# Kernel optimization log

Hardware: AMD Instinct MI355X
Metric: run time of the kernel (lower is better)

The kernel has to match this reference:

```python
import jax, jax.numpy as jnp
import numpy as np

B = 65536          # batch
E = 512            # embedding_dim
SL = 128           # speed_latent_dim
H = 256            # hidden_size
NB = 6             # num_branch
D = E + SL         # 640, branch input dim


def _linear_init(k, din, dout):
    bound = 1.0 / np.sqrt(din)
    kw, kb = jax.random.split(k)
    W = jax.random.uniform(kw, (din, dout), minval=-bound, maxval=bound, dtype=jnp.float32)
    b = jax.random.uniform(kb, (dout,), minval=-bound, maxval=bound, dtype=jnp.float32)
    return W, b


def setup_inputs() -> dict:
    key = jax.random.key(0)
    ks = jax.random.split(key, 10)
    embedding = jax.random.normal(ks[0], (B, E), dtype=jnp.float32)
    speed = jax.random.uniform(ks[1], (B, 1), dtype=jnp.float32)
    command = jax.random.randint(ks[2], (B,), 1, NB + 1)  # values in 1..6

    # speed_in: Linear(1,H) -> ReLU -> Linear(H,SL)
    si_W1, si_b1 = _linear_init(ks[3], 1, H)
    si_W2, si_b2 = _linear_init(ks[4], H, SL)

    # speed_out: Linear(D,H) -> ReLU -> Linear(H,H) -> ReLU -> Linear(H,1)
    so_W1, so_b1 = _linear_init(ks[5], D, H)
    so_W2, so_b2 = _linear_init(ks[6], H, H)
    so_W3, so_b3 = _linear_init(ks[7], H, 1)

    # NB branches, each Linear(D,H)->ReLU->Linear(H,H)->ReLU->Linear(H,3)->Sigmoid
    def mk_branch(k):
        k1, k2, k3 = jax.random.split(k, 3)
        W1, b1 = _linear_init(k1, D, H)
        W2, b2 = _linear_init(k2, H, H)
        W3, b3 = _linear_init(k3, H, 3)
        return W1, b1, W2, b2, W3, b3

    bW1, bb1, bW2, bb2, bW3, bb3 = jax.vmap(mk_branch)(jax.random.split(ks[8], NB))

    return {
        "embedding": embedding, "speed": speed, "command": command,
        "si_W1": si_W1, "si_b1": si_b1, "si_W2": si_W2, "si_b2": si_b2,
        "bW1": bW1, "bb1": bb1, "bW2": bW2, "bb2": bb2, "bW3": bW3, "bb3": bb3,
        "so_W1": so_W1, "so_b1": so_b1, "so_W2": so_W2, "so_b2": so_b2,
        "so_W3": so_W3, "so_b3": so_b3,
    }


def reference(embedding, speed, command,
              si_W1, si_b1, si_W2, si_b2,
              bW1, bb1, bW2, bb2, bW3, bb3,
              so_W1, so_b1, so_W2, so_b2, so_W3, so_b3):
    # speed_in MLP and concat
    s = jax.nn.relu(speed @ si_W1 + si_b1) @ si_W2 + si_b2          # [B, SL]
    emb = jnp.concatenate([embedding, s], axis=1)                    # [B, D]

    # all branches computed densely (as in the torch module), then one-hot mask
    h1 = jax.nn.relu(jnp.einsum('bd,ndh->nbh', emb, bW1) + bb1[:, None, :])   # [NB,B,H]
    h2 = jax.nn.relu(jnp.einsum('nbh,nhk->nbk', h1, bW2) + bb2[:, None, :])   # [NB,B,H]
    out = jax.nn.sigmoid(jnp.einsum('nbk,nko->nbo', h2, bW3) + bb3[:, None, :])  # [NB,B,3]

    mask = (jnp.arange(NB)[:, None] == (command - 1)[None, :]).astype(out.dtype)  # [NB,B]
    control_pred = jnp.sum(out * mask[:, :, None], axis=0)           # [B, 3]

    # speed prediction head
    sp = jax.nn.relu(emb @ so_W1 + so_b1)
    sp = jax.nn.relu(sp @ so_W2 + so_b2)
    speed_pred = sp @ so_W3 + so_b3                                  # [B, 1]

    return control_pred, speed_pred
```

## Files before the change

kernel.cpp:

```cpp
#include <hip/hip_runtime.h>
#include <cstdint>
#include <cstddef>

typedef _Float16 f16;
typedef f16 f16x8 __attribute__((ext_vector_type(8)));
typedef float f32x4 __attribute__((ext_vector_type(4)));

#define B_ROWS 65536
#define TILE_M 128
#define NT_BRANCH 518
#define NT_SPEED 512

constexpr size_t OFF_AF16   = 0;
constexpr size_t SZ_AF16    = (size_t)B_ROWS * 640 * 2;
constexpr size_t OFF_SIW2T  = OFF_AF16 + SZ_AF16;
constexpr size_t SZ_SIW2T   = (size_t)128 * 256 * 2;
constexpr size_t OFF_BW1T   = OFF_SIW2T + SZ_SIW2T;
constexpr size_t SZ_BW1T    = (size_t)6 * 256 * 640 * 2;
constexpr size_t OFF_BW2T   = OFF_BW1T + SZ_BW1T;
constexpr size_t SZ_BW2T    = (size_t)6 * 256 * 256 * 2;
constexpr size_t OFF_SOW1T  = OFF_BW2T + SZ_BW2T;
constexpr size_t SZ_SOW1T   = (size_t)256 * 640 * 2;
constexpr size_t OFF_SOW2T  = OFF_SOW1T + SZ_SOW1T;
constexpr size_t SZ_SOW2T   = (size_t)256 * 256 * 2;
constexpr size_t OFF_BW3T16 = OFF_SOW2T + SZ_SOW2T;
constexpr size_t SZ_BW3T16  = (size_t)6 * 16 * 256 * 2;
constexpr size_t OFF_SOW3T16= OFF_BW3T16 + SZ_BW3T16;
constexpr size_t SZ_SOW3T16 = (size_t)16 * 256 * 2;
constexpr size_t OFF_COUNTS = OFF_SOW3T16 + SZ_SOW3T16;
constexpr size_t OFF_CURSORS= OFF_COUNTS + 256;
constexpr size_t OFF_BINBASE= OFF_CURSORS + 256;
constexpr size_t OFF_TILECMD= OFF_BINBASE + 256;
constexpr size_t OFF_PERM   = OFF_TILECMD + 4352;
constexpr size_t WS_NEEDED  = OFF_PERM + (size_t)NT_BRANCH * TILE_M * 4;

#define MFMA16(a, b, c) __builtin_amdgcn_mfma_f32_16x16x32_f16(a, b, c, 0, 0, 0)
#define BARSYNC() asm volatile("s_waitcnt lgkmcnt(0)\n\ts_barrier" ::: "memory")
#define GLOAD16(gp, lp) __builtin_amdgcn_global_load_lds( \
    (const __attribute__((address_space(1))) void*)(gp),  \
    (__attribute__((address_space(3))) void*)(lp), 16, 0, 0)

__global__ void prep_kernel(const float* __restrict__ siW2,
                            const float* __restrict__ bW1,
                            const float* __restrict__ bW2,
                            const float* __restrict__ soW1,
                            const float* __restrict__ soW2,
                            const float* __restrict__ bW3,
                            const float* __restrict__ soW3,
                            f16* __restrict__ siW2T, f16* __restrict__ bW1T,
                            f16* __restrict__ bW2T, f16* __restrict__ soW1T,
                            f16* __restrict__ soW2T,
                            f16* __restrict__ bW3T16, f16* __restrict__ soW3T16,
                            int* __restrict__ counts, int* __restrict__ cursors,
                            int* __restrict__ perm)
{
    const int bx = blockIdx.x;
    const int tx = threadIdx.x, ty = threadIdx.y;
    const int tid = ty * 32 + tx;
    if (bx >= 1601) {
        const int ib = bx - 1601;
        const int idx = ib * 256 + tid;
        if (idx < NT_BRANCH * TILE_M) perm[idx] = -1;
        if (ib == 0 && tid < 6) { counts[tid] = 0; cursors[tid] = 0; }
        return;
    }
    if (bx == 1600) {
        for (int i = tid; i < 6 * 16 * 256; i += 256) {
            const int c = i >> 12, rem = i & 4095, n = rem >> 8, k = rem & 255;
            bW3T16[i] = (n < 3) ? (f16)bW3[((size_t)c * 256 + k) * 3 + n] : (f16)0;
        }
        for (int i = tid; i < 16 * 256; i += 256) {
            const int n = i >> 8, k = i & 255;
            soW3T16[i] = (n == 0) ? (f16)soW3[k] : (f16)0;
        }
        return;
    }
    const float* in; f16* out; int R, C, lb;
    if (bx < 960)       { int m = bx / 160;        lb = bx - m * 160;       in = bW1 + (size_t)m * 640 * 256; out = bW1T + (size_t)m * 640 * 256; R = 640; C = 256; }
    else if (bx < 1344) { int m = (bx - 960) / 64; lb = (bx - 960) - m * 64; in = bW2 + (size_t)m * 256 * 256; out = bW2T + (size_t)m * 256 * 256; R = 256; C = 256; }
    else if (bx < 1504) { lb = bx - 1344; in = soW1; out = soW1T; R = 640; C = 256; }
    else if (bx < 1568) { lb = bx - 1504; in = soW2; out = soW2T; R = 256; C = 256; }
    else                { lb = bx - 1568; in = siW2; out = siW2T; R = 256; C = 128; }
    const int txt = C >> 5;
    const int c0 = (lb % txt) << 5;
    const int r0 = (lb / txt) << 5;
    __shared__ float tile[32][33];
    #pragma unroll
    for (int i = 0; i < 4; ++i)
        tile[tx][ty + 8 * i] = in[(size_t)(r0 + ty + 8 * i) * C + c0 + tx];
    __syncthreads();
    #pragma unroll
    for (int i = 0; i < 4; ++i)
        out[(size_t)(c0 + ty + 8 * i) * R + r0 + tx] = (f16)tile[ty + 8 * i][tx];
}

__global__ __launch_bounds__(256) void speedin_kernel(
    const float* __restrict__ emb,
    const float* __restrict__ speed,
    const float* __restrict__ siW1, const float* __restrict__ sib1,
    const f16* __restrict__ siW2T, const float* __restrict__ sib2,
    const int* __restrict__ cmd,
    f16* __restrict__ AF16, int* __restrict__ counts)
{
    __shared__ f16 H[64 * 264];
    __shared__ float spd[64];
    __shared__ int h[6];
    const int tid = threadIdx.x;
    const int rb = blockIdx.x * 64;
    if (tid < 6) h[tid] = 0;
    __syncthreads();
    if (tid < 64) {
        spd[tid] = speed[rb + tid];
        atomicAdd(&h[cmd[rb + tid] - 1], 1);
    }
    __syncthreads();
    if (tid < 6 && h[tid] > 0) atomicAdd(&counts[tid], h[tid]);
    {
        const int wv = tid >> 6, ln = tid & 63;
        #pragma unroll 4
        for (int rr = 0; rr < 16; ++rr) {
            const int row = rb + wv * 16 + rr;
            const float* src = emb + (size_t)row * 512 + ln * 8;
            const float4 f0 = ((const float4*)src)[0];
            const float4 f1 = ((const float4*)src)[1];
            f16x8 v;
            v[0] = (f16)f0.x; v[1] = (f16)f0.y; v[2] = (f16)f0.z; v[3] = (f16)f0.w;
            v[4] = (f16)f1.x; v[5] = (f16)f1.y; v[6] = (f16)f1.z; v[7] = (f16)f1.w;
            *(f16x8*)(AF16 + (size_t)row * 640 + ln * 8) = v;
        }
    }
    {
        const float w1 = siW1[tid], b1v = sib1[tid];
        #pragma unroll 4
        for (int r = 0; r < 64; ++r) {
            float hv = spd[r] * w1 + b1v;
            H[r * 264 + tid] = (f16)(hv > 0.f ? hv : 0.f);
        }
    }
    __syncthreads();
    const int w = tid >> 6, lane = tid & 63, lq = lane >> 4, l16 = lane & 15;
    const int nb = w * 32;
    f32x4 acc[4][2];
    #pragma unroll
    for (int mt = 0; mt < 4; ++mt)
        #pragma unroll
        for (int nt = 0; nt < 2; ++nt)
            acc[mt][nt] = (f32x4){0.f, 0.f, 0.f, 0.f};
    for (int ks = 0; ks < 8; ++ks) {
        const int koff = ks * 32 + lq * 8;
        f16x8 af[4], bf[2];
        #pragma unroll
        for (int mt = 0; mt < 4; ++mt)
            af[mt] = *(const f16x8*)(&H[(mt * 16 + l16) * 264 + koff]);
        #pragma unroll
        for (int nt = 0; nt < 2; ++nt)
            bf[nt] = *(const f16x8*)(siW2T + (size_t)(nb + nt * 16 + l16) * 256 + koff);
        #pragma unroll
        for (int mt = 0; mt < 4; ++mt)
            #pragma unroll
            for (int nt = 0; nt < 2; ++nt)
                acc[mt][nt] = MFMA16(af[mt], bf[nt], acc[mt][nt]);
    }
    #pragma unroll
    for (int mt = 0; mt < 4; ++mt)
        #pragma unroll
        for (int nt = 0; nt < 2; ++nt) {
            const int n = nb + nt * 16 + l16;
            const float bv = sib2[n];
            #pragma unroll
            for (int r2 = 0; r2 < 4; ++r2) {
                const int m = mt * 16 + lq * 4 + r2;
                AF16[(size_t)(rb + m) * 640 + 512 + n] = (f16)(acc[mt][nt][r2] + bv);
            }
        }
}

__global__ void plan_kernel(const int* __restrict__ counts,
                            int* __restrict__ binBase, int* __restrict__ tile_cmd) {
    __shared__ int tbase[7];
    if (threadIdx.x == 0) {
        int base = 0, tb = 0;
        for (int c = 0; c < 6; ++c) {
            binBase[c] = base;
            tbase[c] = tb;
            const int nt = (counts[c] + TILE_M - 1) >> 7;
            tb += nt;
            base += nt << 7;
        }
        tbase[6] = tb;
    }
    __syncthreads();
    for (int t = threadIdx.x; t < NT_BRANCH; t += 256) {
        int c = -1;
        #pragma unroll
        for (int j = 0; j < 6; ++j)
            if (t >= tbase[j] && t < tbase[j + 1]) c = j;
        tile_cmd[t] = c;
    }
}

__global__ void place_kernel(const int* __restrict__ cmd,
                             const int* __restrict__ binBase,
                             int* __restrict__ cursors, int* __restrict__ perm) {
    __shared__ int lcnt[6], lbase[6];
    const int tid = threadIdx.x;
    if (tid < 6) lcnt[tid] = 0;
    __syncthreads();
    const int i = blockIdx.x * 256 + tid;
    const int c = cmd[i] - 1;
    const int myr = atomicAdd(&lcnt[c], 1);
    __syncthreads();
    if (tid < 6) lbase[tid] = atomicAdd(&cursors[tid], lcnt[tid]);
    __syncthreads();
    perm[binBase[c] + lbase[c] + myr] = i;
}

__global__ __launch_bounds__(512, 4) void heads_kernel(
    const f16* __restrict__ AF16,
    const int* __restrict__ perm, const int* __restrict__ tile_cmd,
    const f16* __restrict__ bW1T, const f16* __restrict__ bW2T,
    const f16* __restrict__ bW3T16,
    const float* __restrict__ bb1, const float* __restrict__ bb2,
    const float* __restrict__ bb3,
    const f16* __restrict__ soW1T, const f16* __restrict__ soW2T,
    const f16* __restrict__ soW3T16,
    const float* __restrict__ sob1, const float* __restrict__ sob2,
    const float* __restrict__ sob3,
    float* __restrict__ out)
{
    __shared__ f16 smem[33792];
    __shared__ int rowIdx[TILE_M];
    const int bx = blockIdx.x;
    const int tid = threadIdx.x;
    const bool is_speed = (bx >= NT_BRANCH);
    const f16 *W1T, *W2T, *W3T;
    const float *bias1, *bias2, *bias3;
    if (is_speed) {
        const int t = bx - NT_BRANCH;
        if (tid < TILE_M) rowIdx[tid] = t * TILE_M + tid;
        W1T = soW1T; W2T = soW2T; W3T = soW3T16;
        bias1 = sob1; bias2 = sob2; bias3 = sob3;
    } else {
        const int c = tile_cmd[bx];
        if (c < 0) return;
        if (tid < TILE_M) rowIdx[tid] = perm[bx * TILE_M + tid];
        W1T = bW1T + (size_t)c * 256 * 640;
        W2T = bW2T + (size_t)c * 256 * 256;
        W3T = bW3T16 + (size_t)c * 16 * 256;
        bias1 = bb1 + c * 256; bias2 = bb2 + c * 256; bias3 = bb3 + c * 3;
    }
    __syncthreads();

    const int r0 = tid >> 3, j = tid & 7, key = r0 & 7;
    int g0 = rowIdx[r0];      if (g0 < 0) g0 = 0;
    int g1 = rowIdx[r0 + 64]; if (g1 < 0) g1 = 0;
    const f16* srcP0 = AF16 + (size_t)g0 * 640 + (j ^ key) * 8;
    const f16* srcP1 = AF16 + (size_t)g1 * 640 + (j ^ key) * 8;

    const int w = tid >> 6, lane = tid & 63, lq = lane >> 4, l16 = lane & 15;
    const int ldsW = w * 512;
    const int nb = w * 32;
    const f16* brow0 = W1T + (size_t)(nb + l16) * 640;
    const f16* brow1 = W1T + (size_t)(nb + 16 + l16) * 640;

    f32x4 acc[8][2];
    #pragma unroll
    for (int mt = 0; mt < 8; ++mt)
        #pragma unroll
        for (int nt = 0; nt < 2; ++nt)
            acc[mt][nt] = (f32x4){0.f, 0.f, 0.f, 0.f};

    GLOAD16(srcP0,            smem + 0 * 8192 + ldsW);
    GLOAD16(srcP1,            smem + 0 * 8192 + 4096 + ldsW);
    GLOAD16(srcP0 + 64,       smem + 1 * 8192 + ldsW);
    GLOAD16(srcP1 + 64,       smem + 1 * 8192 + 4096 + ldsW);
    asm volatile("s_waitcnt vmcnt(2)\n\ts_barrier" ::: "memory");

    #pragma unroll
    for (int kc = 0; kc < 10; ++kc) {
        const f16* cur = smem + (kc % 3) * 8192;
        f16x8 Bb[2][2];
        #pragma unroll
        for (int ks = 0; ks < 2; ++ks) {
            Bb[ks][0] = *(const f16x8*)(brow0 + kc * 64 + ks * 32 + lq * 8);
            Bb[ks][1] = *(const f16x8*)(brow1 + kc * 64 + ks * 32 + lq * 8);
        }
        if (kc < 8) {
            GLOAD16(srcP0 + (kc + 2) * 64, smem + ((kc + 2) % 3) * 8192 + ldsW);
            GLOAD16(srcP1 + (kc + 2) * 64, smem + ((kc + 2) % 3) * 8192 + 4096 + ldsW);
        }
        #pragma unroll
        for (int ks = 0; ks < 2; ++ks)
            #pragma unroll
            for (int mh = 0; mh < 2; ++mh) {
                f16x8 a[4];
                #pragma unroll
                for (int mt = 0; mt < 4; ++mt) {
                    const int row = mh * 64 + mt * 16 + l16;
                    a[mt] = *(const f16x8*)(cur + row * 64 + ((ks * 4 + lq) ^ (l16 & 7)) * 8);
                }
                #pragma unroll
                for (int mt = 0; mt < 4; ++mt) {
                    acc[mh * 4 + mt][0] = MFMA16(a[mt], Bb[ks][0], acc[mh * 4 + mt][0]);
                    acc[mh * 4 + mt][1] = MFMA16(a[mt], Bb[ks][1], acc[mh * 4 + mt][1]);
                }
            }
        if (kc < 8)
            asm volatile("s_waitcnt vmcnt(2)\n\ts_barrier" ::: "memory");
        else if (kc == 8)
            asm volatile("s_waitcnt vmcnt(4)\n\ts_barrier" ::: "memory");
        else
            BARSYNC();
    }

    const f16* brow2[2];
    #pragma unroll
    for (int nt = 0; nt < 2; ++nt)
        brow2[nt] = W2T + (size_t)(nb + nt * 16 + l16) * 256;
    f16x8 Bd[2][2];
    #pragma unroll
    for (int nt = 0; nt < 2; ++nt)
        Bd[0][nt] = *(const f16x8*)(brow2[nt] + lq * 8);

    #pragma unroll
    for (int mt = 0; mt < 8; ++mt)
        #pragma unroll
        for (int nt = 0; nt < 2; ++nt) {
            const int n = nb + nt * 16 + l16;
            const float bv = bias1[n];
            #pragma unroll
            for (int r2 = 0; r2 < 4; ++r2) {
                const int m = mt * 16 + lq * 4 + r2;
                const float v = acc[mt][nt][r2] + bv;
                smem[m * 264 + n] = (f16)(v > 0.f ? v : 0.f);
            }
            acc[mt][nt] = (f32x4){0.f, 0.f, 0.f, 0.f};
        }
    BARSYNC();

    #pragma unroll
    for (int ks = 0; ks < 8; ++ks) {
        if (ks < 7) {
            #pragma unroll
            for (int nt = 0; nt < 2; ++nt)
                Bd[(ks + 1) & 1][nt] = *(const f16x8*)(brow2[nt] + (ks + 1) * 32 + lq * 8);
        }
        #pragma unroll
        for (int mh = 0; mh < 2; ++mh) {
            f16x8 a[4];
            #pragma unroll
            for (int mt = 0; mt < 4; ++mt)
                a[mt] = *(const f16x8*)(&smem[((mh * 4 + mt) * 16 + l16) * 264 + ks * 32 + lq * 8]);
            #pragma unroll
            for (int mt = 0; mt < 4; ++mt) {
                acc[mh * 4 + mt][0] = MFMA16(a[mt], Bd[ks & 1][0], acc[mh * 4 + mt][0]);
                acc[mh * 4 + mt][1] = MFMA16(a[mt], Bd[ks & 1][1], acc[mh * 4 + mt][1]);
            }
        }
    }
    BARSYNC();
    #pragma unroll
    for (int mt = 0; mt < 8; ++mt)
        #pragma unroll
        for (int nt = 0; nt < 2; ++nt) {
            const int n = nb + nt * 16 + l16;
            const float bv = bias2[n];
            #pragma unroll
            for (int r2 = 0; r2 < 4; ++r2) {
                const int m = mt * 16 + lq * 4 + r2;
                const float v = acc[mt][nt][r2] + bv;
                smem[m * 264 + n] = (f16)(v > 0.f ? v : 0.f);
            }
        }
    BARSYNC();
    {
        f32x4 acc3 = (f32x4){0.f, 0.f, 0.f, 0.f};
        const f16* w3row = W3T + (size_t)l16 * 256;
        #pragma unroll
        for (int ks = 0; ks < 8; ++ks) {
            const int koff = ks * 32 + lq * 8;
            const f16x8 af = *(const f16x8*)(&smem[(w * 16 + l16) * 264 + koff]);
            const f16x8 bf = *(const f16x8*)(w3row + koff);
            acc3 = MFMA16(af, bf, acc3);
        }
        const int orow = w * 16 + lq * 4;
        if (!is_speed) {
            if (l16 < 3) {
                const float b3 = bias3[l16];
                #pragma unroll
                for (int r2 = 0; r2 < 4; ++r2) {
                    const int g = rowIdx[orow + r2];
                    if (g >= 0)
                        out[(size_t)g * 3 + l16] = 1.f / (1.f + __expf(-(acc3[r2] + b3)));
                }
            }
        } else {
            if (l16 == 0) {
                const float b3 = bias3[0];
                #pragma unroll
                for (int r2 = 0; r2 < 4; ++r2) {
                    const int g = rowIdx[orow + r2];
                    if (g >= 0)
                        out[(size_t)3 * B_ROWS + g] = acc3[r2] + b3;
                }
            }
        }
    }
}

extern "C" void kernel_launch(void* const* d_in, const int* in_sizes, int n_in,
                              void* d_out, int out_size, void* d_ws, size_t ws_size,
                              hipStream_t stream) {
    (void)in_sizes; (void)n_in; (void)out_size; (void)ws_size;
    const float* embedding = (const float*)d_in[0];
    const float* speed     = (const float*)d_in[1];
    const int*   command   = (const int*)d_in[2];
    const float* si_W1 = (const float*)d_in[3];
    const float* si_b1 = (const float*)d_in[4];
    const float* si_W2 = (const float*)d_in[5];
    const float* si_b2 = (const float*)d_in[6];
    const float* bW1   = (const float*)d_in[7];
    const float* bb1   = (const float*)d_in[8];
    const float* bW2   = (const float*)d_in[9];
    const float* bb2   = (const float*)d_in[10];
    const float* bW3   = (const float*)d_in[11];
    const float* bb3   = (const float*)d_in[12];
    const float* so_W1 = (const float*)d_in[13];
    const float* so_b1 = (const float*)d_in[14];
    const float* so_W2 = (const float*)d_in[15];
    const float* so_b2 = (const float*)d_in[16];
    const float* so_W3 = (const float*)d_in[17];
    const float* so_b3 = (const float*)d_in[18];
    float* out = (float*)d_out;

    char* ws = (char*)d_ws;
    f16* AF16   = (f16*)(ws + OFF_AF16);
    f16* siW2T  = (f16*)(ws + OFF_SIW2T);
    f16* bW1T   = (f16*)(ws + OFF_BW1T);
    f16* bW2T   = (f16*)(ws + OFF_BW2T);
    f16* soW1T  = (f16*)(ws + OFF_SOW1T);
    f16* soW2T  = (f16*)(ws + OFF_SOW2T);
    f16* bW3T16 = (f16*)(ws + OFF_BW3T16);
    f16* soW3T16= (f16*)(ws + OFF_SOW3T16);
    int* counts = (int*)(ws + OFF_COUNTS);
    int* cursors= (int*)(ws + OFF_CURSORS);
    int* binBase= (int*)(ws + OFF_BINBASE);
    int* tile_cmd = (int*)(ws + OFF_TILECMD);
    int* perm   = (int*)(ws + OFF_PERM);

    prep_kernel<<<1860, dim3(32, 8), 0, stream>>>(
        si_W2, bW1, bW2, so_W1, so_W2, bW3, so_W3,
        siW2T, bW1T, bW2T, soW1T, soW2T, bW3T16, soW3T16,
        counts, cursors, perm);
    speedin_kernel<<<1024, 256, 0, stream>>>(
        embedding, speed, si_W1, si_b1, siW2T, si_b2, command, AF16, counts);
    plan_kernel<<<1, 256, 0, stream>>>(counts, binBase, tile_cmd);
    place_kernel<<<256, 256, 0, stream>>>(command, binBase, cursors, perm);
    heads_kernel<<<NT_BRANCH + NT_SPEED, 512, 0, stream>>>(
        AF16, perm, tile_cmd,
        bW1T, bW2T, bW3T16, bb1, bb2, bb3,
        soW1T, soW2T, soW3T16, so_b1, so_b2, so_b3, out);
}
```

Before: 405.9 us.

## Halve heads tile to 64 rows with 4-stage LDS ring and prefetched weight fragments

```diff
diff --git a/kernel.cpp b/kernel.cpp
--- a/kernel.cpp
+++ b/kernel.cpp
@@ -7,9 +7,9 @@
 typedef float f32x4 __attribute__((ext_vector_type(4)));
 
 #define B_ROWS 65536
-#define TILE_M 128
-#define NT_BRANCH 518
-#define NT_SPEED 512
+#define TILE_M 64
+#define NT_BRANCH 1030
+#define NT_SPEED 1024
 
 constexpr size_t OFF_AF16   = 0;
 constexpr size_t SZ_AF16    = (size_t)B_ROWS * 640 * 2;
@@ -39,6 +39,7 @@
 #define GLOAD16(gp, lp) __builtin_amdgcn_global_load_lds( \
     (const __attribute__((address_space(1))) void*)(gp),  \
     (__attribute__((address_space(3))) void*)(lp), 16, 0, 0)
+#define SCHED_FENCE() __builtin_amdgcn_sched_barrier(0)
 
 __global__ void prep_kernel(const float* __restrict__ siW2,
                             const float* __restrict__ bW1,
@@ -183,9 +184,9 @@
         for (int c = 0; c < 6; ++c) {
             binBase[c] = base;
             tbase[c] = tb;
-            const int nt = (counts[c] + TILE_M - 1) >> 7;
+            const int nt = (counts[c] + 63) >> 6;
             tb += nt;
-            base += nt << 7;
+            base += nt << 6;
         }
         tbase[6] = tb;
     }
@@ -228,7 +229,7 @@
     const float* __restrict__ sob3,
     float* __restrict__ out)
 {
-    __shared__ f16 smem[33792];
+    __shared__ f16 smem[16896];
     __shared__ int rowIdx[TILE_M];
     const int bx = blockIdx.x;
     const int tid = threadIdx.x;
@@ -252,10 +253,8 @@
     __syncthreads();
 
     const int r0 = tid >> 3, j = tid & 7, key = r0 & 7;
-    int g0 = rowIdx[r0];      if (g0 < 0) g0 = 0;
-    int g1 = rowIdx[r0 + 64]; if (g1 < 0) g1 = 0;
-    const f16* srcP0 = AF16 + (size_t)g0 * 640 + (j ^ key) * 8;
-    const f16* srcP1 = AF16 + (size_t)g1 * 640 + (j ^ key) * 8;
+    int g0 = rowIdx[r0]; if (g0 < 0) g0 = 0;
+    const f16* srcP = AF16 + (size_t)g0 * 640 + (j ^ key) * 8;
 
     const int w = tid >> 6, lane = tid & 63, lq = lane >> 4, l16 = lane & 15;
     const int ldsW = w * 512;
@@ -263,54 +262,66 @@
     const f16* brow0 = W1T + (size_t)(nb + l16) * 640;
     const f16* brow1 = W1T + (size_t)(nb + 16 + l16) * 640;
 
-    f32x4 acc[8][2];
-    #pragma unroll
-    for (int mt = 0; mt < 8; ++mt)
+    f32x4 acc[4][2];
+    #pragma unroll
+    for (int mt = 0; mt < 4; ++mt)
         #pragma unroll
         for (int nt = 0; nt < 2; ++nt)
             acc[mt][nt] = (f32x4){0.f, 0.f, 0.f, 0.f};
 
-    GLOAD16(srcP0,            smem + 0 * 8192 + ldsW);
-    GLOAD16(srcP1,            smem + 0 * 8192 + 4096 + ldsW);
-    GLOAD16(srcP0 + 64,       smem + 1 * 8192 + ldsW);
-    GLOAD16(srcP1 + 64,       smem + 1 * 8192 + 4096 + ldsW);
-    asm volatile("s_waitcnt vmcnt(2)\n\ts_barrier" ::: "memory");
+    GLOAD16(srcP,       smem + 0 * 4096 + ldsW);
+    GLOAD16(srcP + 64,  smem + 1 * 4096 + ldsW);
+    GLOAD16(srcP + 128, smem + 2 * 4096 + ldsW);
+    SCHED_FENCE();
+    f16x8 Bb[2][2];
+    #pragma unroll
+    for (int ks = 0; ks < 2; ++ks) {
+        Bb[ks][0] = *(const f16x8*)(brow0 + ks * 32 + lq * 8);
+        Bb[ks][1] = *(const f16x8*)(brow1 + ks * 32 + lq * 8);
+    }
+    SCHED_FENCE();
+    asm volatile("s_waitcnt vmcnt(6)\n\ts_barrier" ::: "memory");
 
     #pragma unroll
     for (int kc = 0; kc < 10; ++kc) {
-        const f16* cur = smem + (kc % 3) * 8192;
-        f16x8 Bb[2][2];
+        const f16* cur = smem + (kc & 3) * 4096;
+        if (kc <= 6) {
+            GLOAD16(srcP + (kc + 3) * 64, smem + ((kc + 3) & 3) * 4096 + ldsW);
+        }
+        SCHED_FENCE();
+        f16x8 Bn[2][2];
+        if (kc <= 8) {
+            #pragma unroll
+            for (int ks = 0; ks < 2; ++ks) {
+                Bn[ks][0] = *(const f16x8*)(brow0 + (kc + 1) * 64 + ks * 32 + lq * 8);
+                Bn[ks][1] = *(const f16x8*)(brow1 + (kc + 1) * 64 + ks * 32 + lq * 8);
+            }
+        }
+        SCHED_FENCE();
         #pragma unroll
         for (int ks = 0; ks < 2; ++ks) {
-            Bb[ks][0] = *(const f16x8*)(brow0 + kc * 64 + ks * 32 + lq * 8);
-            Bb[ks][1] = *(const f16x8*)(brow1 + kc * 64 + ks * 32 + lq * 8);
-        }
-        if (kc < 8) {
-            GLOAD16(srcP0 + (kc + 2) * 64, smem + ((kc + 2) % 3) * 8192 + ldsW);
-            GLOAD16(srcP1 + (kc + 2) * 64, smem + ((kc + 2) % 3) * 8192 + 4096 + ldsW);
-        }
-        #pragma unroll
-        for (int ks = 0; ks < 2; ++ks)
-            #pragma unroll
-            for (int mh = 0; mh < 2; ++mh) {
-                f16x8 a[4];
+            f16x8 a[4];
+            #pragma unroll
+            for (int mt = 0; mt < 4; ++mt)
+                a[mt] = *(const f16x8*)(cur + (mt * 16 + l16) * 64 + ((ks * 4 + lq) ^ (l16 & 7)) * 8);
+            #pragma unroll
+            for (int mt = 0; mt < 4; ++mt) {
+                acc[mt][0] = MFMA16(a[mt], Bb[ks][0], acc[mt][0]);
+                acc[mt][1] = MFMA16(a[mt], Bb[ks][1], acc[mt][1]);
+            }
+        }
+        if (kc <= 8) {
+            #pragma unroll
+            for (int ks = 0; ks < 2; ++ks)
                 #pragma unroll
-                for (int mt = 0; mt < 4; ++mt) {
-                    const int row = mh * 64 + mt * 16 + l16;
-                    a[mt] = *(const f16x8*)(cur + row * 64 + ((ks * 4 + lq) ^ (l16 & 7)) * 8);
-                }
-                #pragma unroll
-                for (int mt = 0; mt < 4; ++mt) {
-                    acc[mh * 4 + mt][0] = MFMA16(a[mt], Bb[ks][0], acc[mh * 4 + mt][0]);
-                    acc[mh * 4 + mt][1] = MFMA16(a[mt], Bb[ks][1], acc[mh * 4 + mt][1]);
-                }
-            }
-        if (kc < 8)
-            asm volatile("s_waitcnt vmcnt(2)\n\ts_barrier" ::: "memory");
-        else if (kc == 8)
-            asm volatile("s_waitcnt vmcnt(4)\n\ts_barrier" ::: "memory");
-        else
-            BARSYNC();
+                for (int nt = 0; nt < 2; ++nt)
+                    Bb[ks][nt] = Bn[ks][nt];
+        }
+        if (kc == 0)      asm volatile("s_waitcnt vmcnt(10)\n\ts_barrier" ::: "memory");
+        else if (kc <= 6) asm volatile("s_waitcnt vmcnt(14)\n\ts_barrier" ::: "memory");
+        else if (kc == 7) asm volatile("s_waitcnt vmcnt(13)\n\ts_barrier" ::: "memory");
+        else if (kc == 8) asm volatile("s_waitcnt vmcnt(12)\n\ts_barrier" ::: "memory");
+        else              BARSYNC();
     }
 
     const f16* brow2[2];
@@ -323,7 +334,7 @@
         Bd[0][nt] = *(const f16x8*)(brow2[nt] + lq * 8);
 
     #pragma unroll
-    for (int mt = 0; mt < 8; ++mt)
+    for (int mt = 0; mt < 4; ++mt)
         #pragma unroll
         for (int nt = 0; nt < 2; ++nt) {
             const int n = nb + nt * 16 + l16;
@@ -345,22 +356,19 @@
             for (int nt = 0; nt < 2; ++nt)
                 Bd[(ks + 1) & 1][nt] = *(const f16x8*)(brow2[nt] + (ks + 1) * 32 + lq * 8);
         }
-        #pragma unroll
-        for (int mh = 0; mh < 2; ++mh) {
-            f16x8 a[4];
-            #pragma unroll
-            for (int mt = 0; mt < 4; ++mt)
-                a[mt] = *(const f16x8*)(&smem[((mh * 4 + mt) * 16 + l16) * 264 + ks * 32 + lq * 8]);
-            #pragma unroll
-            for (int mt = 0; mt < 4; ++mt) {
-                acc[mh * 4 + mt][0] = MFMA16(a[mt], Bd[ks & 1][0], acc[mh * 4 + mt][0]);
-                acc[mh * 4 + mt][1] = MFMA16(a[mt], Bd[ks & 1][1], acc[mh * 4 + mt][1]);
-            }
+        f16x8 a[4];
+        #pragma unroll
+        for (int mt = 0; mt < 4; ++mt)
+            a[mt] = *(const f16x8*)(&smem[(mt * 16 + l16) * 264 + ks * 32 + lq * 8]);
+        #pragma unroll
+        for (int mt = 0; mt < 4; ++mt) {
+            acc[mt][0] = MFMA16(a[mt], Bd[ks & 1][0], acc[mt][0]);
+            acc[mt][1] = MFMA16(a[mt], Bd[ks & 1][1], acc[mt][1]);
         }
     }
     BARSYNC();
     #pragma unroll
-    for (int mt = 0; mt < 8; ++mt)
+    for (int mt = 0; mt < 4; ++mt)
         #pragma unroll
         for (int nt = 0; nt < 2; ++nt) {
             const int n = nb + nt * 16 + l16;
@@ -373,7 +381,7 @@
             }
         }
     BARSYNC();
-    {
+    if (w < 4) {
         f32x4 acc3 = (f32x4){0.f, 0.f, 0.f, 0.f};
         const f16* w3row = W3T + (size_t)l16 * 256;
         #pragma unroll
@@ -448,7 +456,7 @@
     int* tile_cmd = (int*)(ws + OFF_TILECMD);
     int* perm   = (int*)(ws + OFF_PERM);
 
-    prep_kernel<<<1860, dim3(32, 8), 0, stream>>>(
+    prep_kernel<<<1859, dim3(32, 8), 0, stream>>>(
         si_W2, bW1, bW2, so_W1, so_W2, bW3, so_W3,
         siW2T, bW1T, bW2T, soW1T, soW2T, bW3T16, soW3T16,
         counts, cursors, perm);
```

Result: no change. 403.5 us (-0.6%).
